# Optimization experiments

Measured on AMD Instinct MI355X. Metric: run time of the kernel, lower is better.

Reference implementation:

```python
import jax, jax.numpy as jnp
import numpy as np

B = 2048       # batch
POOL = 512     # e_prompt_pool_size
TOPK = 4       # top_k
EPL = 8        # e_prompt_length
GPL = 8        # g_prompt_length
EMB = 768      # emb_d
KEYD = 768     # key_dim


def setup_inputs() -> dict:
    key = jax.random.key(0)
    k1, k2, k3, k4, k5 = jax.random.split(key, 5)
    return {
        "x_querry": jax.random.normal(k1, (B, KEYD), dtype=jnp.float32),
        "x_block": jax.random.normal(k2, (B, EMB), dtype=jnp.float32),
        "e_k": jax.random.uniform(k3, (POOL, KEYD), dtype=jnp.float32),
        "e_p": jax.random.uniform(k4, (POOL, EPL, EMB), dtype=jnp.float32),
        "g_p": jax.random.uniform(k5, (GPL, EMB), dtype=jnp.float32),
        "l": 0,
    }


def _l2norm(x, eps=1e-12):
    # matches torch F.normalize(dim=-1): x / max(||x||, eps)
    n = jnp.sqrt(jnp.sum(x * x, axis=-1, keepdims=True))
    return x / jnp.maximum(n, eps)


def reference(x_querry, x_block, e_k, e_p, g_p, l):
    # ---- E-prompt routing (l in e_layers) ----
    n_K = _l2norm(e_k)                              # [P, C]
    q = jax.lax.stop_gradient(_l2norm(x_querry))    # [B, C], detached in torch
    cos_sim = jnp.einsum('bj,kj->bk', q, n_K)       # [B, P]
    distance = 1.0 - cos_sim
    # use_contrastiv=False -> mass = 1.0
    scaled_distance = distance * 1.0
    # torch.topk(largest=False) == top_k of negated values
    _, k_idx = jax.lax.top_k(-scaled_distance, TOPK)   # [B, K]
    P_ = e_p[k_idx]                                  # [B, K, EPL, EMB] gather
    # non-contrastive loss: (1 - cos_sim[:, k_idx]).mean() -> [B, B, K] mean
    loss = jnp.mean(1.0 - cos_sim[:, k_idx])
    i = EPL // 2
    Ek = P_[:, :, :i, :].reshape(B, -1, EMB)         # [B, K*i, EMB]
    Ev = P_[:, :, i:, :].reshape(B, -1, EMB)
    # count scatter (train_count update)
    counts = jnp.bincount(k_idx.reshape(-1), length=POOL)

    # ---- G-prompt (l in g_layers) ----
    j = GPL // 2
    Gk = jnp.broadcast_to(g_p[:j], (B, j, EMB))
    Gv = jnp.broadcast_to(g_p[j:], (B, GPL - j, EMB))

    Pk = jnp.concatenate([Ek, Gk], axis=1)           # [B, K*i + j, EMB]
    Pv = jnp.concatenate([Ev, Gv], axis=1)
    return Pk, Pv, loss, counts, x_block
```

## Files before the change

kernel.cpp:

```cpp
#include <hip/hip_runtime.h>
#include <hip/hip_bf16.h>
#include <math.h>

static constexpr int NB    = 2048;
static constexpr int NPOOL = 512;
static constexpr int NTOPK = 4;
static constexpr int NEPL  = 8;
static constexpr int NEMB  = 768;
static constexpr int NSLOT = 20;

__global__ __launch_bounds__(256) void norms_kernel(
    const float* __restrict__ xq, const float* __restrict__ ek,
    double* __restrict__ qn, double* __restrict__ kn) {
  int row = blockIdx.x;
  const float* src;
  double* dst;
  if (row < NB) { src = xq + (size_t)row * NEMB; dst = qn + row; }
  else          { src = ek + (size_t)(row - NB) * NEMB; dst = kn + (row - NB); }
  double s = 0.0;
  for (int i = threadIdx.x; i < NEMB; i += 256) {
    double v = (double)src[i];
    s += v * v;
  }
  for (int off = 32; off > 0; off >>= 1) s += __shfl_down(s, off, 64);
  __shared__ double red[4];
  if ((threadIdx.x & 63) == 0) red[threadIdx.x >> 6] = s;
  __syncthreads();
  if (threadIdx.x == 0) *dst = sqrt(red[0] + red[1] + red[2] + red[3]);
}

__global__ __launch_bounds__(256) void cos_kernel(
    const float* __restrict__ xq, const float* __restrict__ ek,
    const double* __restrict__ qn, const double* __restrict__ kn,
    double* __restrict__ cosm) {
  __shared__ double As[32][33];
  __shared__ double Bs[32][33];
  const int tid = threadIdx.x;
  const int tx = tid & 15;
  const int ty = tid >> 4;
  const int bp = blockIdx.x * 32;
  const int bb = blockIdx.y * 32;
  const int lrow = tid >> 3;
  const int lc4  = (tid & 7) * 4;
  double acc00 = 0, acc01 = 0, acc10 = 0, acc11 = 0;
  for (int k0 = 0; k0 < NEMB; k0 += 32) {
    float4 a  = *(const float4*)(xq + (size_t)(bb + lrow) * NEMB + k0 + lc4);
    float4 bv = *(const float4*)(ek + (size_t)(bp + lrow) * NEMB + k0 + lc4);
    As[lrow][lc4 + 0] = (double)a.x;  As[lrow][lc4 + 1] = (double)a.y;
    As[lrow][lc4 + 2] = (double)a.z;  As[lrow][lc4 + 3] = (double)a.w;
    Bs[lrow][lc4 + 0] = (double)bv.x; Bs[lrow][lc4 + 1] = (double)bv.y;
    Bs[lrow][lc4 + 2] = (double)bv.z; Bs[lrow][lc4 + 3] = (double)bv.w;
    __syncthreads();
#pragma unroll
    for (int kk = 0; kk < 32; kk++) {
      double a0 = As[ty * 2][kk],  a1 = As[ty * 2 + 1][kk];
      double b0 = Bs[tx * 2][kk],  b1 = Bs[tx * 2 + 1][kk];
      acc00 = fma(a0, b0, acc00);  acc01 = fma(a0, b1, acc01);
      acc10 = fma(a1, b0, acc10);  acc11 = fma(a1, b1, acc11);
    }
    __syncthreads();
  }
  int b0 = bb + ty * 2, p0 = bp + tx * 2;
  double dq0 = fmax(qn[b0], 1e-12),     dq1 = fmax(qn[b0 + 1], 1e-12);
  double dp0 = fmax(kn[p0], 1e-12),     dp1 = fmax(kn[p0 + 1], 1e-12);
  cosm[(size_t)b0 * NPOOL + p0]           = acc00 / (dq0 * dp0);
  cosm[(size_t)b0 * NPOOL + p0 + 1]       = acc01 / (dq0 * dp1);
  cosm[(size_t)(b0 + 1) * NPOOL + p0]     = acc10 / (dq1 * dp0);
  cosm[(size_t)(b0 + 1) * NPOOL + p0 + 1] = acc11 / (dq1 * dp1);
}

__device__ __forceinline__ bool tk_better(double av, int ai, double bv, int bi) {
  return (av > bv) || (av == bv && ai < bi);
}

__global__ __launch_bounds__(256) void topk_kernel(
    const double* __restrict__ cosm, int* __restrict__ kidx,
    int* __restrict__ counts) {
  int wave = threadIdx.x >> 6, lane = threadIdx.x & 63;
  int row = blockIdx.x * 4 + wave;
  const double* crow = cosm + (size_t)row * NPOOL;
  double v[4] = {-1e300, -1e300, -1e300, -1e300};
  int vi[4] = {0x7fffffff, 0x7fffffff, 0x7fffffff, 0x7fffffff};
#pragma unroll
  for (int j = 0; j < 8; j++) {
    int p = j * 64 + lane;
    double x = crow[p];
    if (x > v[3]) {
      if (x > v[0]) {
        v[3]=v[2]; vi[3]=vi[2]; v[2]=v[1]; vi[2]=vi[1]; v[1]=v[0]; vi[1]=vi[0];
        v[0]=x; vi[0]=p;
      } else if (x > v[1]) {
        v[3]=v[2]; vi[3]=vi[2]; v[2]=v[1]; vi[2]=vi[1]; v[1]=x; vi[1]=p;
      } else if (x > v[2]) {
        v[3]=v[2]; vi[3]=vi[2]; v[2]=x; vi[2]=p;
      } else {
        v[3]=x; vi[3]=p;
      }
    }
  }
#pragma unroll
  for (int off = 1; off < 64; off <<= 1) {
    double ov[4]; int oi[4];
#pragma unroll
    for (int m = 0; m < 4; m++) {
      ov[m] = __shfl_xor(v[m], off, 64);
      oi[m] = __shfl_xor(vi[m], off, 64);
    }
    double mv[4]; int mi[4];
    int ia = 0, ib = 0;
#pragma unroll
    for (int m = 0; m < 4; m++) {
      if (tk_better(v[ia], vi[ia], ov[ib], oi[ib])) { mv[m]=v[ia]; mi[m]=vi[ia]; ia++; }
      else                                          { mv[m]=ov[ib]; mi[m]=oi[ib]; ib++; }
    }
#pragma unroll
    for (int m = 0; m < 4; m++) { v[m] = mv[m]; vi[m] = mi[m]; }
  }
  if (lane == 0) {
#pragma unroll
    for (int m = 0; m < 4; m++) {
      kidx[row * 4 + m] = vi[m];
      atomicAdd(&counts[vi[m]], 1);
    }
  }
}

__global__ __launch_bounds__(256) void colsum_kernel(
    const double* __restrict__ cosm, double* __restrict__ S) {
  int p = blockIdx.x * 256 + threadIdx.x;
  int r0 = blockIdx.y * 128;
  double s = 0.0;
  for (int r = r0; r < r0 + 128; r++) s += cosm[(size_t)r * NPOOL + p];
  atomicAdd(&S[p], s);
}

__global__ __launch_bounds__(256) void loss_counts_kernel(
    const double* __restrict__ S, const int* __restrict__ counts,
    float* __restrict__ out_loss, float* __restrict__ out_counts) {
  double s = 0.0;
  for (int p = threadIdx.x; p < NPOOL; p += 256) {
    int c = counts[p];
    out_counts[p] = (float)c;
    s += (double)c * S[p];
  }
  for (int off = 32; off > 0; off >>= 1) s += __shfl_down(s, off, 64);
  __shared__ double red[4];
  if ((threadIdx.x & 63) == 0) red[threadIdx.x >> 6] = s;
  __syncthreads();
  if (threadIdx.x == 0) {
    double total = red[0] + red[1] + red[2] + red[3];
    *out_loss = (float)(1.0 - total / (double)((long long)NB * NB * NTOPK));
  }
}

__global__ __launch_bounds__(256) void gather_kernel(
    const float* __restrict__ e_p, const float* __restrict__ g_p,
    const int* __restrict__ kidx, float* __restrict__ Pk,
    float* __restrict__ Pv) {
  int b = blockIdx.x;
  __shared__ int idx[4];
  if (threadIdx.x < 4) idx[threadIdx.x] = kidx[b * 4 + threadIdx.x];
  __syncthreads();
  float4* dk = (float4*)(Pk + (size_t)b * NSLOT * NEMB);
  float4* dv = (float4*)(Pv + (size_t)b * NSLOT * NEMB);
  const int R = NEMB / 4;
  for (int u = threadIdx.x; u < NSLOT * R; u += 256) {
    int s = u / R;
    int r = u - s * R;
    const float4* sk;
    const float4* sv;
    if (s < 16) {
      int pi = idx[s >> 2];
      int t = s & 3;
      const float* basek = e_p + ((size_t)pi * NEPL + t) * NEMB;
      sk = (const float4*)basek;
      sv = (const float4*)(basek + 4 * NEMB);
    } else {
      sk = (const float4*)(g_p + (size_t)(s - 16) * NEMB);
      sv = (const float4*)(g_p + (size_t)(s - 16 + 4) * NEMB);
    }
    dk[u] = sk[r];
    dv[u] = sv[r];
  }
}

__global__ __launch_bounds__(256) void copy_kernel(
    const float* __restrict__ src, float* __restrict__ dst, int n) {
  int i = blockIdx.x * 256 + threadIdx.x;
  int stride = gridDim.x * 256;
  for (; i < n; i += stride) dst[i] = src[i];
}

extern "C" void kernel_launch(void* const* d_in, const int* in_sizes, int n_in,
                              void* d_out, int out_size, void* d_ws, size_t ws_size,
                              hipStream_t stream) {
  const float* x_querry = (const float*)d_in[0];
  const float* x_block  = (const float*)d_in[1];
  const float* e_k      = (const float*)d_in[2];
  const float* e_p      = (const float*)d_in[3];
  const float* g_p      = (const float*)d_in[4];

  double* qn     = (double*)d_ws;
  double* kn     = qn + NB;
  double* S      = kn + NPOOL;
  double* cosm   = S + NPOOL;
  int*    kidx   = (int*)(cosm + (size_t)NB * NPOOL);
  int*    counts = kidx + NB * NTOPK;

  float* out        = (float*)d_out;
  float* Pk         = out;
  float* Pv         = Pk + (size_t)NB * NSLOT * NEMB;
  float* out_loss   = Pv + (size_t)NB * NSLOT * NEMB;
  float* out_counts = out_loss + 1;
  float* out_xb     = out_counts + NPOOL;

  hipMemsetAsync(S, 0, NPOOL * sizeof(double), stream);
  hipMemsetAsync(counts, 0, NPOOL * sizeof(int), stream);

  norms_kernel<<<NB + NPOOL, 256, 0, stream>>>(x_querry, e_k, qn, kn);
  cos_kernel<<<dim3(NPOOL / 32, NB / 32), 256, 0, stream>>>(x_querry, e_k, qn, kn, cosm);
  topk_kernel<<<NB / 4, 256, 0, stream>>>(cosm, kidx, counts);
  colsum_kernel<<<dim3(NPOOL / 256, NB / 128), 256, 0, stream>>>(cosm, S);
  loss_counts_kernel<<<1, 256, 0, stream>>>(S, counts, out_loss, out_counts);
  gather_kernel<<<NB, 256, 0, stream>>>(e_p, g_p, kidx, Pk, Pv);
  copy_kernel<<<1024, 256, 0, stream>>>(x_block, out_xb, NB * NEMB);
}
```

Measured before the change: 437.5 us.

## Compute cosine matrix in fp32 with double-precision rerank of top-8 candidates

Switches the similarity GEMM from fp64 to fp32 with a 64x64 register-blocked tile and precomputed reciprocal norms, and stores the cosine matrix as float. Top-k now keeps 8 candidates via a sorting network and bitonic wave merge, then recomputes those 8 dot products in double precision to pick the final top-4. This removes slow fp64 FMA throughput and halves the cosine matrix traffic, at the risk of candidate misses if fp32 error exceeds the top-8 margin. The x_block copy is also folded into the gather kernel to save a launch.

Result: faster. 381.9 us (-12.7%).

```diff
diff --git a/kernel.cpp b/kernel.cpp
--- a/kernel.cpp
+++ b/kernel.cpp
@@ -8,15 +8,18 @@
 static constexpr int NEPL  = 8;
 static constexpr int NEMB  = 768;
 static constexpr int NSLOT = 20;
+static constexpr int NCAND = 8;
 
 __global__ __launch_bounds__(256) void norms_kernel(
     const float* __restrict__ xq, const float* __restrict__ ek,
-    double* __restrict__ qn, double* __restrict__ kn) {
+    double* __restrict__ qn, double* __restrict__ kn,
+    float* __restrict__ rqn, float* __restrict__ rkn) {
   int row = blockIdx.x;
   const float* src;
   double* dst;
-  if (row < NB) { src = xq + (size_t)row * NEMB; dst = qn + row; }
-  else          { src = ek + (size_t)(row - NB) * NEMB; dst = kn + (row - NB); }
+  float* rdst;
+  if (row < NB) { src = xq + (size_t)row * NEMB; dst = qn + row; rdst = rqn + row; }
+  else          { src = ek + (size_t)(row - NB) * NEMB; dst = kn + (row - NB); rdst = rkn + (row - NB); }
   double s = 0.0;
   for (int i = threadIdx.x; i < NEMB; i += 256) {
     double v = (double)src[i];
@@ -26,111 +29,156 @@
   __shared__ double red[4];
   if ((threadIdx.x & 63) == 0) red[threadIdx.x >> 6] = s;
   __syncthreads();
-  if (threadIdx.x == 0) *dst = sqrt(red[0] + red[1] + red[2] + red[3]);
+  if (threadIdx.x == 0) {
+    double n = sqrt(red[0] + red[1] + red[2] + red[3]);
+    *dst = n;
+    *rdst = (float)(1.0 / fmax(n, 1e-12));
+  }
 }
 
 __global__ __launch_bounds__(256) void cos_kernel(
     const float* __restrict__ xq, const float* __restrict__ ek,
-    const double* __restrict__ qn, const double* __restrict__ kn,
-    double* __restrict__ cosm) {
-  __shared__ double As[32][33];
-  __shared__ double Bs[32][33];
-  const int tid = threadIdx.x;
-  const int tx = tid & 15;
-  const int ty = tid >> 4;
-  const int bp = blockIdx.x * 32;
-  const int bb = blockIdx.y * 32;
-  const int lrow = tid >> 3;
-  const int lc4  = (tid & 7) * 4;
-  double acc00 = 0, acc01 = 0, acc10 = 0, acc11 = 0;
+    const float* __restrict__ rqn, const float* __restrict__ rkn,
+    float* __restrict__ cosm) {
+  __shared__ float As[32][68];
+  __shared__ float Bs[32][68];
+  const int t = threadIdx.x;
+  const int tx = t & 15;
+  const int ty = t >> 4;
+  const int bp = blockIdx.x * 64;
+  const int bb = blockIdx.y * 64;
+  float acc[4][4] = {};
   for (int k0 = 0; k0 < NEMB; k0 += 32) {
-    float4 a  = *(const float4*)(xq + (size_t)(bb + lrow) * NEMB + k0 + lc4);
-    float4 bv = *(const float4*)(ek + (size_t)(bp + lrow) * NEMB + k0 + lc4);
-    As[lrow][lc4 + 0] = (double)a.x;  As[lrow][lc4 + 1] = (double)a.y;
-    As[lrow][lc4 + 2] = (double)a.z;  As[lrow][lc4 + 3] = (double)a.w;
-    Bs[lrow][lc4 + 0] = (double)bv.x; Bs[lrow][lc4 + 1] = (double)bv.y;
-    Bs[lrow][lc4 + 2] = (double)bv.z; Bs[lrow][lc4 + 3] = (double)bv.w;
+#pragma unroll
+    for (int uu = 0; uu < 2; uu++) {
+      int u = t + uu * 256;
+      int m = u >> 3;
+      int k4 = (u & 7) * 4;
+      float4 a = *(const float4*)(xq + (size_t)(bb + m) * NEMB + k0 + k4);
+      float4 b = *(const float4*)(ek + (size_t)(bp + m) * NEMB + k0 + k4);
+      As[k4 + 0][m] = a.x; As[k4 + 1][m] = a.y; As[k4 + 2][m] = a.z; As[k4 + 3][m] = a.w;
+      Bs[k4 + 0][m] = b.x; Bs[k4 + 1][m] = b.y; Bs[k4 + 2][m] = b.z; Bs[k4 + 3][m] = b.w;
+    }
     __syncthreads();
 #pragma unroll
     for (int kk = 0; kk < 32; kk++) {
-      double a0 = As[ty * 2][kk],  a1 = As[ty * 2 + 1][kk];
-      double b0 = Bs[tx * 2][kk],  b1 = Bs[tx * 2 + 1][kk];
-      acc00 = fma(a0, b0, acc00);  acc01 = fma(a0, b1, acc01);
-      acc10 = fma(a1, b0, acc10);  acc11 = fma(a1, b1, acc11);
+      float4 av = *(const float4*)&As[kk][ty * 4];
+      float4 bv = *(const float4*)&Bs[kk][tx * 4];
+      acc[0][0] = fmaf(av.x, bv.x, acc[0][0]); acc[0][1] = fmaf(av.x, bv.y, acc[0][1]);
+      acc[0][2] = fmaf(av.x, bv.z, acc[0][2]); acc[0][3] = fmaf(av.x, bv.w, acc[0][3]);
+      acc[1][0] = fmaf(av.y, bv.x, acc[1][0]); acc[1][1] = fmaf(av.y, bv.y, acc[1][1]);
+      acc[1][2] = fmaf(av.y, bv.z, acc[1][2]); acc[1][3] = fmaf(av.y, bv.w, acc[1][3]);
+      acc[2][0] = fmaf(av.z, bv.x, acc[2][0]); acc[2][1] = fmaf(av.z, bv.y, acc[2][1]);
+      acc[2][2] = fmaf(av.z, bv.z, acc[2][2]); acc[2][3] = fmaf(av.z, bv.w, acc[2][3]);
+      acc[3][0] = fmaf(av.w, bv.x, acc[3][0]); acc[3][1] = fmaf(av.w, bv.y, acc[3][1]);
+      acc[3][2] = fmaf(av.w, bv.z, acc[3][2]); acc[3][3] = fmaf(av.w, bv.w, acc[3][3]);
     }
     __syncthreads();
   }
-  int b0 = bb + ty * 2, p0 = bp + tx * 2;
-  double dq0 = fmax(qn[b0], 1e-12),     dq1 = fmax(qn[b0 + 1], 1e-12);
-  double dp0 = fmax(kn[p0], 1e-12),     dp1 = fmax(kn[p0 + 1], 1e-12);
-  cosm[(size_t)b0 * NPOOL + p0]           = acc00 / (dq0 * dp0);
-  cosm[(size_t)b0 * NPOOL + p0 + 1]       = acc01 / (dq0 * dp1);
-  cosm[(size_t)(b0 + 1) * NPOOL + p0]     = acc10 / (dq1 * dp0);
-  cosm[(size_t)(b0 + 1) * NPOOL + p0 + 1] = acc11 / (dq1 * dp1);
-}
-
-__device__ __forceinline__ bool tk_better(double av, int ai, double bv, int bi) {
+  float4 rk = *(const float4*)&rkn[bp + tx * 4];
+#pragma unroll
+  for (int i = 0; i < 4; i++) {
+    float rq = rqn[bb + ty * 4 + i];
+    float4 cv;
+    cv.x = acc[i][0] * rq * rk.x;
+    cv.y = acc[i][1] * rq * rk.y;
+    cv.z = acc[i][2] * rq * rk.z;
+    cv.w = acc[i][3] * rq * rk.w;
+    *(float4*)(cosm + (size_t)(bb + ty * 4 + i) * NPOOL + bp + tx * 4) = cv;
+  }
+}
+
+__device__ __forceinline__ bool btf(float av, int ai, float bv, int bi) {
   return (av > bv) || (av == bv && ai < bi);
 }
+__device__ __forceinline__ bool btd(double av, int ai, double bv, int bi) {
+  return (av > bv) || (av == bv && ai < bi);
+}
+#define CE(a, b)                                                        \
+  do {                                                                  \
+    if (!btf(v[a], vi[a], v[b], vi[b])) {                               \
+      float tv = v[a]; v[a] = v[b]; v[b] = tv;                          \
+      int ti = vi[a]; vi[a] = vi[b]; vi[b] = ti;                        \
+    }                                                                   \
+  } while (0)
 
 __global__ __launch_bounds__(256) void topk_kernel(
-    const double* __restrict__ cosm, int* __restrict__ kidx,
+    const float* __restrict__ cosm, const float* __restrict__ xq,
+    const float* __restrict__ ek, const double* __restrict__ qn,
+    const double* __restrict__ kn, int* __restrict__ kidx,
     int* __restrict__ counts) {
   int wave = threadIdx.x >> 6, lane = threadIdx.x & 63;
   int row = blockIdx.x * 4 + wave;
-  const double* crow = cosm + (size_t)row * NPOOL;
-  double v[4] = {-1e300, -1e300, -1e300, -1e300};
-  int vi[4] = {0x7fffffff, 0x7fffffff, 0x7fffffff, 0x7fffffff};
+  const float* crow = cosm + (size_t)row * NPOOL;
+  float v[8]; int vi[8];
 #pragma unroll
   for (int j = 0; j < 8; j++) {
     int p = j * 64 + lane;
-    double x = crow[p];
-    if (x > v[3]) {
-      if (x > v[0]) {
-        v[3]=v[2]; vi[3]=vi[2]; v[2]=v[1]; vi[2]=vi[1]; v[1]=v[0]; vi[1]=vi[0];
-        v[0]=x; vi[0]=p;
-      } else if (x > v[1]) {
-        v[3]=v[2]; vi[3]=vi[2]; v[2]=v[1]; vi[2]=vi[1]; v[1]=x; vi[1]=p;
-      } else if (x > v[2]) {
-        v[3]=v[2]; vi[3]=vi[2]; v[2]=x; vi[2]=p;
-      } else {
-        v[3]=x; vi[3]=p;
-      }
-    }
-  }
+    v[j] = crow[p];
+    vi[j] = p;
+  }
+  CE(0,1); CE(2,3); CE(4,5); CE(6,7);
+  CE(0,2); CE(1,3); CE(4,6); CE(5,7);
+  CE(1,2); CE(5,6);
+  CE(0,4); CE(1,5); CE(2,6); CE(3,7);
+  CE(2,4); CE(3,5);
+  CE(1,2); CE(3,4); CE(5,6);
 #pragma unroll
   for (int off = 1; off < 64; off <<= 1) {
-    double ov[4]; int oi[4];
-#pragma unroll
-    for (int m = 0; m < 4; m++) {
+    float ov[8]; int oi[8];
+#pragma unroll
+    for (int m = 0; m < 8; m++) {
       ov[m] = __shfl_xor(v[m], off, 64);
       oi[m] = __shfl_xor(vi[m], off, 64);
     }
-    double mv[4]; int mi[4];
-    int ia = 0, ib = 0;
-#pragma unroll
-    for (int m = 0; m < 4; m++) {
-      if (tk_better(v[ia], vi[ia], ov[ib], oi[ib])) { mv[m]=v[ia]; mi[m]=vi[ia]; ia++; }
-      else                                          { mv[m]=ov[ib]; mi[m]=oi[ib]; ib++; }
-    }
-#pragma unroll
-    for (int m = 0; m < 4; m++) { v[m] = mv[m]; vi[m] = mi[m]; }
-  }
-  if (lane == 0) {
-#pragma unroll
-    for (int m = 0; m < 4; m++) {
-      kidx[row * 4 + m] = vi[m];
-      atomicAdd(&counts[vi[m]], 1);
-    }
-  }
-}
+#pragma unroll
+    for (int m = 0; m < 8; m++) {
+      if (!btf(v[m], vi[m], ov[7 - m], oi[7 - m])) { v[m] = ov[7 - m]; vi[m] = oi[7 - m]; }
+    }
+    CE(0,4); CE(1,5); CE(2,6); CE(3,7);
+    CE(0,2); CE(1,3); CE(4,6); CE(5,7);
+    CE(0,1); CE(2,3); CE(4,5); CE(6,7);
+  }
+  const float* xrow = xq + (size_t)row * NEMB;
+  double xr[12];
+#pragma unroll
+  for (int e = 0; e < 12; e++) xr[e] = (double)xrow[lane * 12 + e];
+  double qmax = fmax(qn[row], 1e-12);
+  double cand[8];
+#pragma unroll
+  for (int c = 0; c < 8; c++) {
+    int pi = vi[c];
+    const float* kb = ek + (size_t)pi * NEMB + lane * 12;
+    double s = 0.0;
+#pragma unroll
+    for (int e = 0; e < 12; e++) s = fma(xr[e], (double)kb[e], s);
+#pragma unroll
+    for (int off = 1; off < 64; off <<= 1) s += __shfl_xor(s, off, 64);
+    cand[c] = s / (qmax * fmax(kn[pi], 1e-12));
+  }
+  bool used[8] = {false, false, false, false, false, false, false, false};
+#pragma unroll
+  for (int m = 0; m < NTOPK; m++) {
+    int best = -1;
+#pragma unroll
+    for (int c = 0; c < 8; c++) {
+      if (!used[c] && (best < 0 || btd(cand[c], vi[c], cand[best], vi[best]))) best = c;
+    }
+    used[best] = true;
+    if (lane == 0) {
+      kidx[row * 4 + m] = vi[best];
+      atomicAdd(&counts[vi[best]], 1);
+    }
+  }
+}
+#undef CE
 
 __global__ __launch_bounds__(256) void colsum_kernel(
-    const double* __restrict__ cosm, double* __restrict__ S) {
+    const float* __restrict__ cosm, double* __restrict__ S) {
   int p = blockIdx.x * 256 + threadIdx.x;
   int r0 = blockIdx.y * 128;
   double s = 0.0;
-  for (int r = r0; r < r0 + 128; r++) s += cosm[(size_t)r * NPOOL + p];
+  for (int r = r0; r < r0 + 128; r++) s += (double)cosm[(size_t)r * NPOOL + p];
   atomicAdd(&S[p], s);
 }
 
@@ -155,8 +203,9 @@
 
 __global__ __launch_bounds__(256) void gather_kernel(
     const float* __restrict__ e_p, const float* __restrict__ g_p,
-    const int* __restrict__ kidx, float* __restrict__ Pk,
-    float* __restrict__ Pv) {
+    const int* __restrict__ kidx, const float* __restrict__ x_block,
+    float* __restrict__ Pk, float* __restrict__ Pv,
+    float* __restrict__ out_xb) {
   int b = blockIdx.x;
   __shared__ int idx[4];
   if (threadIdx.x < 4) idx[threadIdx.x] = kidx[b * 4 + threadIdx.x];
@@ -182,13 +231,8 @@
     dk[u] = sk[r];
     dv[u] = sv[r];
   }
-}
-
-__global__ __launch_bounds__(256) void copy_kernel(
-    const float* __restrict__ src, float* __restrict__ dst, int n) {
-  int i = blockIdx.x * 256 + threadIdx.x;
-  int stride = gridDim.x * 256;
-  for (; i < n; i += stride) dst[i] = src[i];
+  for (int i = threadIdx.x; i < NEMB; i += 256)
+    out_xb[(size_t)b * NEMB + i] = x_block[(size_t)b * NEMB + i];
 }
 
 extern "C" void kernel_launch(void* const* d_in, const int* in_sizes, int n_in,
@@ -203,7 +247,9 @@
   double* qn     = (double*)d_ws;
   double* kn     = qn + NB;
   double* S      = kn + NPOOL;
-  double* cosm   = S + NPOOL;
+  float*  rqn    = (float*)(S + NPOOL);
+  float*  rkn    = rqn + NB;
+  float*  cosm   = rkn + NPOOL;
   int*    kidx   = (int*)(cosm + (size_t)NB * NPOOL);
   int*    counts = kidx + NB * NTOPK;
 
@@ -217,11 +263,10 @@
   hipMemsetAsync(S, 0, NPOOL * sizeof(double), stream);
   hipMemsetAsync(counts, 0, NPOOL * sizeof(int), stream);
 
-  norms_kernel<<<NB + NPOOL, 256, 0, stream>>>(x_querry, e_k, qn, kn);
-  cos_kernel<<<dim3(NPOOL / 32, NB / 32), 256, 0, stream>>>(x_querry, e_k, qn, kn, cosm);
-  topk_kernel<<<NB / 4, 256, 0, stream>>>(cosm, kidx, counts);
+  norms_kernel<<<NB + NPOOL, 256, 0, stream>>>(x_querry, e_k, qn, kn, rqn, rkn);
+  cos_kernel<<<dim3(NPOOL / 64, NB / 64), 256, 0, stream>>>(x_querry, e_k, rqn, rkn, cosm);
+  topk_kernel<<<NB / 4, 256, 0, stream>>>(cosm, x_querry, e_k, qn, kn, kidx, counts);
   colsum_kernel<<<dim3(NPOOL / 256, NB / 128), 256, 0, stream>>>(cosm, S);
   loss_counts_kernel<<<1, 256, 0, stream>>>(S, counts, out_loss, out_counts);
-  gather_kernel<<<NB, 256, 0, stream>>>(e_p, g_p, kidx, Pk, Pv);
-  copy_kernel<<<1024, 256, 0, stream>>>(x_block, out_xb, NB * NEMB);
-}
+  gather_kernel<<<NB, 256, 0, stream>>>(e_p, g_p, kidx, x_block, Pk, Pv, out_xb);
+}
```
